# Optimization experiments

Hardware: AMD Instinct MI355X
Metric: run time of the kernel (lower is better)

The kernel has to match this reference:

```python
import jax, jax.numpy as jnp
import numpy as np

B, N, D, H, C = 16, 512, 256, 8, 16
DK = D // H  # per-head dim


def gelu(x):
    return jax.nn.gelu(x, approximate=False)  # torch F.gelu default (erf)


def mha(x, Wq, Wk, Wv, Wo):
    # x: [N, D] treated as a length-N token sequence; standard scaled-dot MHA
    n = x.shape[0]
    q = (x @ Wq).reshape(n, H, DK)
    k = (x @ Wk).reshape(n, H, DK)
    v = (x @ Wv).reshape(n, H, DK)
    scores = jnp.einsum('nhd,mhd->hnm', q, k) / jnp.sqrt(jnp.asarray(DK, x.dtype))
    attn = jax.nn.softmax(scores, axis=-1)
    out = jnp.einsum('hnm,mhd->nhd', attn, v).reshape(n, H * DK)
    return out @ Wo


def setup_inputs() -> dict:
    key = jax.random.key(0)
    ks = jax.random.split(key, 16)
    scale = 1.0 / np.sqrt(D)
    w = lambda i, shape: jax.random.normal(ks[i], shape, jnp.float32) * scale
    return {
        'embeddings': jax.random.normal(ks[0], (B, N, D), jnp.float32),
        'labels': jax.random.randint(ks[1], (B, N), 0, C),
        'Wq0': w(2, (D, D)), 'Wk0': w(3, (D, D)), 'Wv0': w(4, (D, D)), 'Wo0': w(5, (D, D)),
        'Wq1': w(6, (D, D)), 'Wk1': w(7, (D, D)), 'Wv1': w(8, (D, D)), 'Wo1': w(9, (D, D)),
        'res_W': w(10, (D, D)), 'res_b': jnp.zeros((D,), jnp.float32),
        'ff_W1': w(11, (2 * D, D)), 'ff_b1': jnp.zeros((D,), jnp.float32),
        'ff_W2': w(12, (D, D)), 'ff_b2': jnp.zeros((D,), jnp.float32),
    }


def reference(embeddings, labels, Wq0, Wk0, Wv0, Wo0, Wq1, Wk1, Wv1, Wo1,
              res_W, res_b, ff_W1, ff_b1, ff_W2, ff_b2):
    # one-hot class membership; torch.unique over randint labels == arange(C)
    onehot = (labels[..., None] == jnp.arange(C)).astype(jnp.float32)  # [B,N,C]

    def episode(e, m):
        # e: [N, D]  m: [N, C]
        x = mha(e, Wq0, Wk0, Wv0, Wo0)
        x = gelu(x)
        x = mha(x, Wq1, Wk1, Wv1, Wo1)
        aggr = gelu(jnp.mean(x, axis=0))          # [D]  set-level summary
        aggr = aggr @ res_W + res_b               # res_linear
        e2 = jnp.concatenate([jnp.broadcast_to(aggr, (N, D)), e], axis=1)  # [N,2D]
        e2 = gelu(e2)
        e2 = gelu(e2 @ ff_W1 + ff_b1) @ ff_W2 + ff_b2  # ff_linear -> [N,D]
        # pairwise sample similarities with self-exclusion
        S = e2 @ e2.T                              # [N,N]
        S = S * (1.0 - jnp.eye(N, dtype=S.dtype))
        counts = jnp.sum(m, axis=0)                # [C]
        norm = counts[None, :] - m                 # leave-one-out class size [N,C]
        return (S.T @ m) / norm                    # per-class masked mean -> [N,C]

    return jax.vmap(episode)(embeddings, onehot)
```

## Files before the change

kernel.cpp:

```cpp
#include <hip/hip_runtime.h>

#define BB 16
#define NN 512
#define DD 256
#define HH 8
#define CC 16

typedef unsigned short u16;
using short8 = __attribute__((ext_vector_type(8))) short;
using f32x4  = __attribute__((ext_vector_type(4))) float;

__device__ __forceinline__ float gelu_f(float x) {
    return 0.5f * x * (1.0f + erff(x * 0.70710678118654752f));
}
__device__ __forceinline__ u16 f2bf(float f) {
    unsigned int u = __float_as_uint(f);
    unsigned int r = u + 0x7FFFu + ((u >> 16) & 1u);
    return (u16)(r >> 16);
}
__device__ __forceinline__ void gld16(const u16* g, const u16* l) {
    __builtin_amdgcn_global_load_lds(
        (const __attribute__((address_space(1))) unsigned int*)g,
        (__attribute__((address_space(3))) unsigned int*)l, 16, 0, 0);
}

#define QSCALE 0.25505412f

template<int ACT, int HAS_B, int HAS_T, int OUT_F32>
__global__ __launch_bounds__(256) void gemm64(
    const u16* __restrict__ A, const u16* __restrict__ W,
    u16* __restrict__ O, float* __restrict__ OF,
    const float* __restrict__ bias, const float* __restrict__ tvec)
{
    __shared__ __align__(16) u16 As[64 * 32];
    __shared__ __align__(16) u16 Bs[64 * 32];
    const int tid = threadIdx.x, wave = tid >> 6, lane = tid & 63;
    const int col = lane & 15, quad = lane >> 4;
    const int mbase = blockIdx.x * 64;
    const int nbase = blockIdx.y * 64;
    const int srow = lane >> 2, skk = (lane & 3) * 8;
    const int mh = (wave & 1) * 32, nh = (wave >> 1) * 32;

    f32x4 acc[2][2];
#pragma unroll
    for (int i = 0; i < 2; ++i)
#pragma unroll
        for (int j = 0; j < 2; ++j) acc[i][j] = (f32x4){0.f, 0.f, 0.f, 0.f};

    for (int k0 = 0; k0 < DD; k0 += 32) {
        gld16(A + (size_t)(mbase + wave * 16 + srow) * DD + k0 + skk, &As[wave * 512]);
        gld16(W + (size_t)(nbase + wave * 16 + srow) * DD + k0 + skk, &Bs[wave * 512]);
        __syncthreads();
        short8 af[2], bfr[2];
#pragma unroll
        for (int i = 0; i < 2; ++i) af[i]  = *(const short8*)&As[(mh + i * 16 + col) * 32 + quad * 8];
#pragma unroll
        for (int j = 0; j < 2; ++j) bfr[j] = *(const short8*)&Bs[(nh + j * 16 + col) * 32 + quad * 8];
#pragma unroll
        for (int i = 0; i < 2; ++i)
#pragma unroll
            for (int j = 0; j < 2; ++j)
                acc[i][j] = __builtin_amdgcn_mfma_f32_16x16x32_bf16(af[i], bfr[j], acc[i][j], 0, 0, 0);
        __syncthreads();
    }

    const int b = mbase >> 9;
#pragma unroll
    for (int i = 0; i < 2; ++i) {
#pragma unroll
        for (int j = 0; j < 2; ++j) {
            const int ccol = nbase + nh + j * 16 + col;
#pragma unroll
            for (int r = 0; r < 4; ++r) {
                const int crow = mbase + mh + i * 16 + quad * 4 + r;
                float v = acc[i][j][r];
                if (HAS_B) v += bias[ccol];
                if (HAS_T) v += tvec[b * DD + ccol];
                if (ACT)   v = gelu_f(v);
                if (OUT_F32) OF[(size_t)crow * DD + ccol] = v;
                else         O[(size_t)crow * DD + ccol] = f2bf(v);
            }
        }
    }
}

__global__ __launch_bounds__(256) void gemm_qkv(
    const u16* __restrict__ A,
    const u16* __restrict__ W0, const u16* __restrict__ W1, const u16* __restrict__ W2,
    u16* __restrict__ O0, u16* __restrict__ O1, u16* __restrict__ O2)
{
    __shared__ __align__(16) u16 As[64 * 32];
    __shared__ __align__(16) u16 Bs[64 * 32];
    const int tid = threadIdx.x, wave = tid >> 6, lane = tid & 63;
    const int col = lane & 15, quad = lane >> 4;
    const int mbase = blockIdx.x * 64;
    const int sel = blockIdx.y >> 2;
    const int nbase = (blockIdx.y & 3) * 64;
    const u16* W = (sel == 0) ? W0 : ((sel == 1) ? W1 : W2);
    u16* O = (sel == 0) ? O0 : ((sel == 1) ? O1 : O2);
    const int srow = lane >> 2, skk = (lane & 3) * 8;
    const int mh = (wave & 1) * 32, nh = (wave >> 1) * 32;

    f32x4 acc[2][2];
#pragma unroll
    for (int i = 0; i < 2; ++i)
#pragma unroll
        for (int j = 0; j < 2; ++j) acc[i][j] = (f32x4){0.f, 0.f, 0.f, 0.f};

    for (int k0 = 0; k0 < DD; k0 += 32) {
        gld16(A + (size_t)(mbase + wave * 16 + srow) * DD + k0 + skk, &As[wave * 512]);
        gld16(W + (size_t)(nbase + wave * 16 + srow) * DD + k0 + skk, &Bs[wave * 512]);
        __syncthreads();
        short8 af[2], bfr[2];
#pragma unroll
        for (int i = 0; i < 2; ++i) af[i]  = *(const short8*)&As[(mh + i * 16 + col) * 32 + quad * 8];
#pragma unroll
        for (int j = 0; j < 2; ++j) bfr[j] = *(const short8*)&Bs[(nh + j * 16 + col) * 32 + quad * 8];
#pragma unroll
        for (int i = 0; i < 2; ++i)
#pragma unroll
            for (int j = 0; j < 2; ++j)
                acc[i][j] = __builtin_amdgcn_mfma_f32_16x16x32_bf16(af[i], bfr[j], acc[i][j], 0, 0, 0);
        __syncthreads();
    }

    const int b = mbase >> 9;
#pragma unroll
    for (int i = 0; i < 2; ++i) {
#pragma unroll
        for (int j = 0; j < 2; ++j) {
            const int ccol = nbase + nh + j * 16 + col;
            const int tok0 = (mbase & 511) + mh + i * 16 + quad * 4;
            const int head = ccol >> 5, dk = ccol & 31;
            if (sel == 2) {
                ushort4 pk;
                pk.x = f2bf(acc[i][j][0]); pk.y = f2bf(acc[i][j][1]);
                pk.z = f2bf(acc[i][j][2]); pk.w = f2bf(acc[i][j][3]);
                *(ushort4*)&O[(((size_t)b * HH + head) * 32 + dk) * NN + tok0] = pk;
            } else {
#pragma unroll
                for (int r = 0; r < 4; ++r) {
                    float v = acc[i][j][r];
                    if (sel == 0) v *= QSCALE;
                    O[(((size_t)b * HH + head) * NN + tok0 + r) * 32 + dk] = f2bf(v);
                }
            }
        }
    }
}

template<int COLSUM>
__global__ __launch_bounds__(256) void attn_mfma(
    const u16* __restrict__ Qh, const u16* __restrict__ Kh,
    const u16* __restrict__ VT, u16* __restrict__ O,
    float* __restrict__ partial)
{
    __shared__ __align__(16) u16 Vt[32 * 520];
    __shared__ __align__(16) u16 Pc[4][16 * 32];
    __shared__ float cs[4][32];
    const int tid = threadIdx.x, wave = tid >> 6, lane = tid & 63;
    const int col = lane & 15, quad = lane >> 4;
    const int gid = blockIdx.x;
    const int qb = gid >> 7, bh = gid & 127;
    const int q0 = qb * 64 + wave * 16;

    const u16* vsrc = VT + (size_t)bh * 32 * NN;
#pragma unroll
    for (int i = 0; i < 8; ++i) {
        const int row = wave + i * 4;
        gld16(vsrc + (size_t)row * NN + lane * 8, &Vt[row * 520]);
    }
    const short8 aq = *(const short8*)(Qh + ((size_t)bh * NN + q0 + col) * 32 + quad * 8);
    __syncthreads();

    const u16* ksrc = Kh + (size_t)bh * NN * 32;
    float l[4] = {0.f, 0.f, 0.f, 0.f};
    f32x4 oacc[2];
    oacc[0] = (f32x4){0.f, 0.f, 0.f, 0.f};
    oacc[1] = (f32x4){0.f, 0.f, 0.f, 0.f};

    for (int g = 0; g < 16; ++g) {
#pragma unroll
        for (int k2 = 0; k2 < 2; ++k2) {
            const int kt = g * 2 + k2;
            const short8 bk = *(const short8*)(ksrc + (size_t)(kt * 16 + col) * 32 + quad * 8);
            f32x4 z = {0.f, 0.f, 0.f, 0.f};
            const f32x4 s = __builtin_amdgcn_mfma_f32_16x16x32_bf16(aq, bk, z, 0, 0, 0);
#pragma unroll
            for (int r = 0; r < 4; ++r) {
                const float p = exp2f(s[r]);
                l[r] += p;
                Pc[wave][(quad * 4 + r) * 32 + k2 * 16 + col] = f2bf(p);
            }
        }
        const short8 ap = *(const short8*)&Pc[wave][col * 32 + quad * 8];
#pragma unroll
        for (int nt = 0; nt < 2; ++nt) {
            const short8 bv = *(const short8*)&Vt[(nt * 16 + col) * 520 + g * 32 + quad * 8];
            oacc[nt] = __builtin_amdgcn_mfma_f32_16x16x32_bf16(ap, bv, oacc[nt], 0, 0, 0);
        }
    }
#pragma unroll
    for (int r = 0; r < 4; ++r) {
        l[r] += __shfl_xor(l[r], 1, 64);
        l[r] += __shfl_xor(l[r], 2, 64);
        l[r] += __shfl_xor(l[r], 4, 64);
        l[r] += __shfl_xor(l[r], 8, 64);
    }
    if (COLSUM) {
        float sv[2] = {0.f, 0.f};
#pragma unroll
        for (int nt = 0; nt < 2; ++nt) {
#pragma unroll
            for (int r = 0; r < 4; ++r) sv[nt] += oacc[nt][r] / l[r];
            sv[nt] += __shfl_xor(sv[nt], 16, 64);
            sv[nt] += __shfl_xor(sv[nt], 32, 64);
        }
        if (lane < 16) { cs[wave][col] = sv[0]; cs[wave][16 + col] = sv[1]; }
        __syncthreads();
        if (tid < 32)
            partial[(size_t)(bh * 8 + qb) * 32 + tid] =
                cs[0][tid] + cs[1][tid] + cs[2][tid] + cs[3][tid];
    } else {
        const int b = bh >> 3, h = bh & 7;
        u16* obase = O + ((size_t)b * NN) * DD + h * 32;
#pragma unroll
        for (int nt = 0; nt < 2; ++nt)
#pragma unroll
            for (int r = 0; r < 4; ++r)
                obase[(size_t)(q0 + quad * 4 + r) * DD + nt * 16 + col] = f2bf(oacc[nt][r] / l[r]);
    }
}

__global__ __launch_bounds__(256) void convert_all(
    const float* __restrict__ e, u16* __restrict__ E, u16* __restrict__ G,
    const float* s0, const float* s1, const float* s2, const float* s3,
    const float* s4, const float* s5, const float* s6, const float* s7,
    const float* s8, u16* __restrict__ Wt)
{
    const int bx = blockIdx.x;
    if (bx < 2048) {
        const size_t i = ((size_t)bx * 256 + threadIdx.x) * 4;
        const float4 v = *(const float4*)(e + i);
        ushort4 ev, gv;
        ev.x = f2bf(v.x); ev.y = f2bf(v.y); ev.z = f2bf(v.z); ev.w = f2bf(v.w);
        gv.x = f2bf(gelu_f(v.x)); gv.y = f2bf(gelu_f(v.y));
        gv.z = f2bf(gelu_f(v.z)); gv.w = f2bf(gelu_f(v.w));
        *(ushort4*)(E + i) = ev;
        *(ushort4*)(G + i) = gv;
    } else {
        const int w = bx - 2048;
        const int my = w >> 4, kb = (w & 15) * 16;
        const int n = threadIdx.x;
        const float* S;
        switch (my) {
            case 0: S = s0; break; case 1: S = s1; break; case 2: S = s2; break;
            case 3: S = s3; break; case 4: S = s4; break; case 5: S = s5; break;
            case 6: S = s6; break; case 7: S = s7; break; default: S = s8; break;
        }
        u16* Dst = Wt + (size_t)my * 65536;
        for (int r = 0; r < 16; ++r) {
            const int k = kb + r;
            Dst[(size_t)n * 256 + k] = f2bf(S[(size_t)k * 256 + n]);
        }
    }
}

__device__ __forceinline__ float mv256(const float* __restrict__ a,
                                       const float* __restrict__ W, int d)
{
    float acc[8] = {0.f, 0.f, 0.f, 0.f, 0.f, 0.f, 0.f, 0.f};
    for (int k = 0; k < 256; k += 8) {
#pragma unroll
        for (int j = 0; j < 8; ++j)
            acc[j] += a[k + j] * W[(size_t)(k + j) * 256 + d];
    }
    return ((acc[0] + acc[1]) + (acc[2] + acc[3])) + ((acc[4] + acc[5]) + (acc[6] + acc[7]));
}

__global__ __launch_bounds__(256) void aggr_v2(
    const float* __restrict__ partial, const float* __restrict__ Wo1f,
    const float* __restrict__ resW, const float* __restrict__ resb,
    const float* __restrict__ W1, const int* __restrict__ labels,
    float* __restrict__ tvec, float* __restrict__ counts)
{
    const int b = blockIdx.x, d = threadIdx.x;
    __shared__ float a0[256], a1[256], a2[256];
    __shared__ int hist[CC];
    if (d < CC) hist[d] = 0;
    const int h = d >> 5, d32 = d & 31;
    float s = 0.f;
#pragma unroll
    for (int qb = 0; qb < 8; ++qb)
        s += partial[(size_t)(((b * 8 + h) * 8) + qb) * 32 + d32];
    a0[d] = s * (1.0f / NN);
    __syncthreads();
    atomicAdd(&hist[labels[b * NN + d]], 1);
    atomicAdd(&hist[labels[b * NN + 256 + d]], 1);
    a1[d] = gelu_f(mv256(a0, Wo1f, d));
    __syncthreads();
    a2[d] = gelu_f(mv256(a1, resW, d) + resb[d]);
    __syncthreads();
    tvec[b * 256 + d] = mv256(a2, W1, d);
    if (d < CC) counts[b * CC + d] = (float)hist[d];
}

__global__ __launch_bounds__(256) void classsum_v2(
    const float* __restrict__ F, const int* __restrict__ labels,
    float* __restrict__ g)
{
    const int b = blockIdx.x, dch = blockIdx.y;
    const int t = threadIdx.x, w = t >> 6, lane = t & 63;
    __shared__ int lab[NN];
    __shared__ float gs[4][CC][64];
    lab[t] = labels[b * NN + t];
    lab[t + 256] = labels[b * NN + t + 256];
    __syncthreads();
    float acc[CC];
#pragma unroll
    for (int c = 0; c < CC; ++c) acc[c] = 0.f;
    const float* Fb = F + (size_t)b * NN * DD + dch * 64 + lane;
#pragma unroll 4
    for (int n = w * 128; n < w * 128 + 128; ++n) {
        const float v = Fb[(size_t)n * DD];
        const int lb = lab[n];
#pragma unroll
        for (int c = 0; c < CC; ++c) acc[c] += (lb == c) ? v : 0.f;
    }
#pragma unroll
    for (int c = 0; c < CC; ++c) gs[w][c][lane] = acc[c];
    __syncthreads();
#pragma unroll
    for (int i = 0; i < 4; ++i) {
        const int c = w * 4 + i;
        g[((size_t)b * CC + c) * DD + dch * 64 + lane] =
            gs[0][c][lane] + gs[1][c][lane] + gs[2][c][lane] + gs[3][c][lane];
    }
}

__global__ __launch_bounds__(256) void out_kernel(
    const float* __restrict__ F, const int* __restrict__ labels,
    const float* __restrict__ g, const float* __restrict__ counts,
    float* __restrict__ out)
{
    const int b = blockIdx.y;
    const int wave = threadIdx.x >> 6, lane = threadIdx.x & 63;
    const int n = blockIdx.x * 4 + wave;
    const float* fn = F + ((size_t)b * NN + n) * DD;
    const float* gb = g + (size_t)b * CC * DD;
    float fv[4];
#pragma unroll
    for (int i = 0; i < 4; ++i) fv[i] = fn[lane * 4 + i];
    float selfdot = 0.f;
#pragma unroll
    for (int i = 0; i < 4; ++i) selfdot += fv[i] * fv[i];
    float accs[CC];
#pragma unroll
    for (int c = 0; c < CC; ++c) {
        float sacc = 0.f;
#pragma unroll
        for (int i = 0; i < 4; ++i) sacc += fv[i] * gb[c * DD + lane * 4 + i];
        accs[c] = sacc;
    }
    for (int off = 32; off; off >>= 1) {
        selfdot += __shfl_xor(selfdot, off, 64);
#pragma unroll
        for (int c = 0; c < CC; ++c) accs[c] += __shfl_xor(accs[c], off, 64);
    }
    if (lane < CC) {
        const int c = lane;
        const int same = (labels[b * NN + n] == c) ? 1 : 0;
        const float num = accs[c] - (same ? selfdot : 0.f);
        const float den = counts[b * CC + c] - (float)same;
        out[((size_t)b * NN + n) * CC + c] = num / den;
    }
}

extern "C" void kernel_launch(void* const* d_in, const int* in_sizes, int n_in,
                              void* d_out, int out_size, void* d_ws, size_t ws_size,
                              hipStream_t stream)
{
    const float* emb    = (const float*)d_in[0];
    const int*   labels = (const int*)  d_in[1];
    const float* Wo1f = (const float*)d_in[9];
    const float* resW = (const float*)d_in[10];
    const float* resb = (const float*)d_in[11];
    const float* ffW1 = (const float*)d_in[12];
    const float* ffb1 = (const float*)d_in[13];
    const float* ffb2 = (const float*)d_in[15];
    float* out = (float*)d_out;

    const size_t SBE = (size_t)BB * NN * DD;
    u16* BUF0 = (u16*)d_ws;
    u16* BUF1 = BUF0 + SBE;
    u16* BUF2 = BUF1 + SBE;
    u16* BUF3 = BUF2 + SBE;
    u16* BUF4 = BUF3 + SBE;
    u16* BUF5 = BUF4 + SBE;
    u16* Wt   = BUF5 + SBE;
    float* F      = (float*)(Wt + 9 * 65536);
    float* tvec   = F + SBE;
    float* partial= tvec + BB * 256;
    float* gsum   = partial + 128 * 8 * 32;
    float* counts = gsum + (size_t)BB * CC * DD;

    convert_all<<<2048 + 144, 256, 0, stream>>>(
        emb, BUF0, BUF1,
        (const float*)d_in[2], (const float*)d_in[3], (const float*)d_in[4],
        (const float*)d_in[5], (const float*)d_in[6], (const float*)d_in[7],
        (const float*)d_in[8], ffW1 + 256 * 256, (const float*)d_in[14], Wt);
    gemm_qkv<<<dim3(128, 12), 256, 0, stream>>>(
        BUF0, Wt, Wt + 65536, Wt + 2 * 65536, BUF2, BUF3, BUF4);
    attn_mfma<0><<<1024, 256, 0, stream>>>(BUF2, BUF3, BUF4, BUF5, nullptr);
    gemm64<1,0,0,0><<<dim3(128, 4), 256, 0, stream>>>(
        BUF5, Wt + 3 * 65536, BUF0, nullptr, nullptr, nullptr);
    gemm_qkv<<<dim3(128, 12), 256, 0, stream>>>(
        BUF0, Wt + 4 * 65536, Wt + 5 * 65536, Wt + 6 * 65536, BUF2, BUF3, BUF4);
    attn_mfma<1><<<1024, 256, 0, stream>>>(BUF2, BUF3, BUF4, nullptr, partial);
    aggr_v2<<<BB, 256, 0, stream>>>(partial, Wo1f, resW, resb, ffW1, labels, tvec, counts);
    gemm64<1,1,1,0><<<dim3(128, 4), 256, 0, stream>>>(
        BUF1, Wt + 7 * 65536, BUF3, nullptr, ffb1, tvec);
    gemm64<0,1,0,1><<<dim3(128, 4), 256, 0, stream>>>(
        BUF3, Wt + 8 * 65536, nullptr, F, ffb2, nullptr);
    classsum_v2<<<dim3(BB, 4), 256, 0, stream>>>(F, labels, gsum);
    out_kernel<<<dim3(128, BB), 256, 0, stream>>>(F, labels, gsum, counts, out);
}
```

Baseline: 213.0 us.

## Fuse aggregation into attention tail and class sums into FF2 GEMM epilogue

```diff
diff --git a/kernel.cpp b/kernel.cpp
--- a/kernel.cpp
+++ b/kernel.cpp
@@ -26,11 +26,24 @@
 
 #define QSCALE 0.25505412f
 
-template<int ACT, int HAS_B, int HAS_T, int OUT_F32>
+__device__ __forceinline__ float mv256(const float* __restrict__ a,
+                                       const float* __restrict__ W, int d)
+{
+    float acc[8] = {0.f, 0.f, 0.f, 0.f, 0.f, 0.f, 0.f, 0.f};
+    for (int k = 0; k < 256; k += 8) {
+#pragma unroll
+        for (int j = 0; j < 8; ++j)
+            acc[j] += a[k + j] * W[(size_t)(k + j) * 256 + d];
+    }
+    return ((acc[0] + acc[1]) + (acc[2] + acc[3])) + ((acc[4] + acc[5]) + (acc[6] + acc[7]));
+}
+
+template<int ACT, int HAS_B, int HAS_T, int OUT_F32, int CS>
 __global__ __launch_bounds__(256) void gemm64(
     const u16* __restrict__ A, const u16* __restrict__ W,
     u16* __restrict__ O, float* __restrict__ OF,
-    const float* __restrict__ bias, const float* __restrict__ tvec)
+    const float* __restrict__ bias, const float* __restrict__ tvec,
+    const int* __restrict__ labels, float* __restrict__ gsum)
 {
     __shared__ __align__(16) u16 As[64 * 32];
     __shared__ __align__(16) u16 Bs[64 * 32];
@@ -65,21 +78,66 @@
     }
 
     const int b = mbase >> 9;
-#pragma unroll
-    for (int i = 0; i < 2; ++i) {
-#pragma unroll
-        for (int j = 0; j < 2; ++j) {
-            const int ccol = nbase + nh + j * 16 + col;
-#pragma unroll
-            for (int r = 0; r < 4; ++r) {
-                const int crow = mbase + mh + i * 16 + quad * 4 + r;
-                float v = acc[i][j][r];
-                if (HAS_B) v += bias[ccol];
-                if (HAS_T) v += tvec[b * DD + ccol];
-                if (ACT)   v = gelu_f(v);
-                if (OUT_F32) OF[(size_t)crow * DD + ccol] = v;
-                else         O[(size_t)crow * DD + ccol] = f2bf(v);
+    if constexpr (!CS) {
+#pragma unroll
+        for (int i = 0; i < 2; ++i) {
+#pragma unroll
+            for (int j = 0; j < 2; ++j) {
+                const int ccol = nbase + nh + j * 16 + col;
+#pragma unroll
+                for (int r = 0; r < 4; ++r) {
+                    const int crow = mbase + mh + i * 16 + quad * 4 + r;
+                    float v = acc[i][j][r];
+                    if (HAS_B) v += bias[ccol];
+                    if (HAS_T) v += tvec[b * DD + ccol];
+                    if (ACT)   v = gelu_f(v);
+                    if (OUT_F32) OF[(size_t)crow * DD + ccol] = v;
+                    else         O[(size_t)crow * DD + ccol] = f2bf(v);
+                }
             }
+        }
+    } else {
+        __shared__ float Fs[64][65];
+        __shared__ float gs[4][CC][64];
+        __shared__ int lab2[64];
+        if (tid < 64) lab2[tid] = labels[mbase + tid];
+#pragma unroll
+        for (int i = 0; i < 2; ++i) {
+#pragma unroll
+            for (int j = 0; j < 2; ++j) {
+                const int lcol = nh + j * 16 + col;
+                const int ccol = nbase + lcol;
+#pragma unroll
+                for (int r = 0; r < 4; ++r) {
+                    const int lrow = mh + i * 16 + quad * 4 + r;
+                    float v = acc[i][j][r];
+                    if (HAS_B) v += bias[ccol];
+                    if (HAS_T) v += tvec[b * DD + ccol];
+                    if (ACT)   v = gelu_f(v);
+                    OF[(size_t)(mbase + lrow) * DD + ccol] = v;
+                    Fs[lrow][lcol] = v;
+                }
+            }
+        }
+        __syncthreads();
+        float a[CC];
+#pragma unroll
+        for (int c = 0; c < CC; ++c) a[c] = 0.f;
+#pragma unroll
+        for (int n = 0; n < 16; ++n) {
+            const float v = Fs[wave * 16 + n][lane];
+            const int lb = lab2[wave * 16 + n];
+#pragma unroll
+            for (int c = 0; c < CC; ++c) a[c] += (lb == c) ? v : 0.f;
+        }
+#pragma unroll
+        for (int c = 0; c < CC; ++c) gs[wave][c][lane] = a[c];
+        __syncthreads();
+#pragma unroll
+        for (int i = 0; i < 4; ++i) {
+            const int c = wave * 4 + i;
+            atomicAdd(&gsum[((size_t)b * CC + c) * DD + nbase + lane],
+                      gs[0][c][lane] + gs[1][c][lane] + gs[2][c][lane] + gs[3][c][lane]);
         }
     }
 }
@@ -153,7 +211,11 @@
 __global__ __launch_bounds__(256) void attn_mfma(
     const u16* __restrict__ Qh, const u16* __restrict__ Kh,
     const u16* __restrict__ VT, u16* __restrict__ O,
-    float* __restrict__ partial)
+    float* __restrict__ partial,
+    const float* __restrict__ Wo1f, const float* __restrict__ resW,
+    const float* __restrict__ resb, const float* __restrict__ W1,
+    const int* __restrict__ labels, float* __restrict__ tvec,
+    float* __restrict__ counts, int* __restrict__ flags)
 {
     __shared__ __align__(16) u16 Vt[32 * 520];
     __shared__ __align__(16) u16 Pc[4][16 * 32];
@@ -218,9 +280,38 @@
         }
         if (lane < 16) { cs[wave][col] = sv[0]; cs[wave][16 + col] = sv[1]; }
         __syncthreads();
+        const int b = bh >> 3;
         if (tid < 32)
             partial[(size_t)(bh * 8 + qb) * 32 + tid] =
                 cs[0][tid] + cs[1][tid] + cs[2][tid] + cs[3][tid];
+        __threadfence();
+        __syncthreads();
+        __shared__ int isLast;
+        if (tid == 0) isLast = (atomicAdd(&flags[b], 1) == 63);
+        __syncthreads();
+        if (!isLast) return;
+        __threadfence();
+        float* a0 = (float*)Vt;
+        float* a1 = a0 + 256;
+        float* a2 = a1 + 256;
+        int* hist = (int*)(a2 + 256);
+        const int d = tid;
+        if (d < CC) hist[d] = 0;
+        const int hh = d >> 5, d32 = d & 31;
+        float s = 0.f;
+#pragma unroll
+        for (int q8 = 0; q8 < 8; ++q8)
+            s += partial[(size_t)(((b * 8 + hh) * 8) + q8) * 32 + d32];
+        a0[d] = s * (1.0f / NN);
+        __syncthreads();
+        atomicAdd(&hist[labels[b * NN + d]], 1);
+        atomicAdd(&hist[labels[b * NN + 256 + d]], 1);
+        a1[d] = gelu_f(mv256(a0, Wo1f, d));
+        __syncthreads();
+        a2[d] = gelu_f(mv256(a1, resW, d) + resb[d]);
+        __syncthreads();
+        tvec[b * 256 + d] = mv256(a2, W1, d);
+        if (d < CC) counts[b * CC + d] = (float)hist[d];
     } else {
         const int b = bh >> 3, h = bh & 7;
         u16* obase = O + ((size_t)b * NN) * DD + h * 32;
@@ -236,7 +327,8 @@
     const float* __restrict__ e, u16* __restrict__ E, u16* __restrict__ G,
     const float* s0, const float* s1, const float* s2, const float* s3,
     const float* s4, const float* s5, const float* s6, const float* s7,
-    const float* s8, u16* __restrict__ Wt)
+    const float* s8, u16* __restrict__ Wt,
+    float* __restrict__ gsum, int* __restrict__ flags)
 {
     const int bx = blockIdx.x;
     if (bx < 2048) {
@@ -248,7 +340,7 @@
         gv.z = f2bf(gelu_f(v.z)); gv.w = f2bf(gelu_f(v.w));
         *(ushort4*)(E + i) = ev;
         *(ushort4*)(G + i) = gv;
-    } else {
+    } else if (bx < 2192) {
         const int w = bx - 2048;
         const int my = w >> 4, kb = (w & 15) * 16;
         const int n = threadIdx.x;
@@ -263,78 +355,11 @@
             const int k = kb + r;
             Dst[(size_t)n * 256 + k] = f2bf(S[(size_t)k * 256 + n]);
         }
-    }
-}
-
-__device__ __forceinline__ float mv256(const float* __restrict__ a,
-                                       const float* __restrict__ W, int d)
-{
-    float acc[8] = {0.f, 0.f, 0.f, 0.f, 0.f, 0.f, 0.f, 0.f};
-    for (int k = 0; k < 256; k += 8) {
-#pragma unroll
-        for (int j = 0; j < 8; ++j)
-            acc[j] += a[k + j] * W[(size_t)(k + j) * 256 + d];
-    }
-    return ((acc[0] + acc[1]) + (acc[2] + acc[3])) + ((acc[4] + acc[5]) + (acc[6] + acc[7]));
-}
-
-__global__ __launch_bounds__(256) void aggr_v2(
-    const float* __restrict__ partial, const float* __restrict__ Wo1f,
-    const float* __restrict__ resW, const float* __restrict__ resb,
-    const float* __restrict__ W1, const int* __restrict__ labels,
-    float* __restrict__ tvec, float* __restrict__ counts)
-{
-    const int b = blockIdx.x, d = threadIdx.x;
-    __shared__ float a0[256], a1[256], a2[256];
-    __shared__ int hist[CC];
-    if (d < CC) hist[d] = 0;
-    const int h = d >> 5, d32 = d & 31;
-    float s = 0.f;
-#pragma unroll
-    for (int qb = 0; qb < 8; ++qb)
-        s += partial[(size_t)(((b * 8 + h) * 8) + qb) * 32 + d32];
-    a0[d] = s * (1.0f / NN);
-    __syncthreads();
-    atomicAdd(&hist[labels[b * NN + d]], 1);
-    atomicAdd(&hist[labels[b * NN + 256 + d]], 1);
-    a1[d] = gelu_f(mv256(a0, Wo1f, d));
-    __syncthreads();
-    a2[d] = gelu_f(mv256(a1, resW, d) + resb[d]);
-    __syncthreads();
-    tvec[b * 256 + d] = mv256(a2, W1, d);
-    if (d < CC) counts[b * CC + d] = (float)hist[d];
-}
-
-__global__ __launch_bounds__(256) void classsum_v2(
-    const float* __restrict__ F, const int* __restrict__ labels,
-    float* __restrict__ g)
-{
-    const int b = blockIdx.x, dch = blockIdx.y;
-    const int t = threadIdx.x, w = t >> 6, lane = t & 63;
-    __shared__ int lab[NN];
-    __shared__ float gs[4][CC][64];
-    lab[t] = labels[b * NN + t];
-    lab[t + 256] = labels[b * NN + t + 256];
-    __syncthreads();
-    float acc[CC];
-#pragma unroll
-    for (int c = 0; c < CC; ++c) acc[c] = 0.f;
-    const float* Fb = F + (size_t)b * NN * DD + dch * 64 + lane;
-#pragma unroll 4
-    for (int n = w * 128; n < w * 128 + 128; ++n) {
-        const float v = Fb[(size_t)n * DD];
-        const int lb = lab[n];
-#pragma unroll
-        for (int c = 0; c < CC; ++c) acc[c] += (lb == c) ? v : 0.f;
-    }
-#pragma unroll
-    for (int c = 0; c < CC; ++c) gs[w][c][lane] = acc[c];
-    __syncthreads();
-#pragma unroll
-    for (int i = 0; i < 4; ++i) {
-        const int c = w * 4 + i;
-        g[((size_t)b * CC + c) * DD + dch * 64 + lane] =
-            gs[0][c][lane] + gs[1][c][lane] + gs[2][c][lane] + gs[3][c][lane];
+    } else {
+        const int z = bx - 2192;
+        const float4 zz = {0.f, 0.f, 0.f, 0.f};
+        *(float4*)(gsum + (size_t)z * 1024 + threadIdx.x * 4) = zz;
+        if (z == 0 && threadIdx.x < BB) flags[threadIdx.x] = 0;
     }
 }
 
@@ -403,25 +428,29 @@
     float* partial= tvec + BB * 256;
     float* gsum   = partial + 128 * 8 * 32;
     float* counts = gsum + (size_t)BB * CC * DD;
-
-    convert_all<<<2048 + 144, 256, 0, stream>>>(
+    int*   flags  = (int*)(counts + BB * CC);
+
+    convert_all<<<2048 + 144 + 64, 256, 0, stream>>>(
         emb, BUF0, BUF1,
         (const float*)d_in[2], (const float*)d_in[3], (const float*)d_in[4],
         (const float*)d_in[5], (const float*)d_in[6], (const float*)d_in[7],
-        (const float*)d_in[8], ffW1 + 256 * 256, (const float*)d_in[14], Wt);
+        (const float*)d_in[8], ffW1 + 256 * 256, (const float*)d_in[14], Wt,
+        gsum, flags);
     gemm_qkv<<<dim3(128, 12), 256, 0, stream>>>(
         BUF0, Wt, Wt + 65536, Wt + 2 * 65536, BUF2, BUF3, BUF4);
-    attn_mfma<0><<<1024, 256, 0, stream>>>(BUF2, BUF3, BUF4, BUF5, nullptr);
-    gemm64<1,0,0,0><<<dim3(128, 4), 256, 0, stream>>>(
-        BUF5, Wt + 3 * 65536, BUF0, nullptr, nullptr, nullptr);
+    attn_mfma<0><<<1024, 256, 0, stream>>>(
+        BUF2, BUF3, BUF4, BUF5, nullptr,
+        nullptr, nullptr, nullptr, nullptr, nullptr, nullptr, nullptr, nullptr);
+    gemm64<1,0,0,0,0><<<dim3(128, 4), 256, 0, stream>>>(
+        BUF5, Wt + 3 * 65536, BUF0, nullptr, nullptr, nullptr, nullptr, nullptr);
     gemm_qkv<<<dim3(128, 12), 256, 0, stream>>>(
         BUF0, Wt + 4 * 65536, Wt + 5 * 65536, Wt + 6 * 65536, BUF2, BUF3, BUF4);
-    attn_mfma<1><<<1024, 256, 0, stream>>>(BUF2, BUF3, BUF4, nullptr, partial);
-    aggr_v2<<<BB, 256, 0, stream>>>(partial, Wo1f, resW, resb, ffW1, labels, tvec, counts);
-    gemm64<1,1,1,0><<<dim3(128, 4), 256, 0, stream>>>(
-        BUF1, Wt + 7 * 65536, BUF3, nullptr, ffb1, tvec);
-    gemm64<0,1,0,1><<<dim3(128, 4), 256, 0, stream>>>(
-        BUF3, Wt + 8 * 65536, nullptr, F, ffb2, nullptr);
-    classsum_v2<<<dim3(BB, 4), 256, 0, stream>>>(F, labels, gsum);
+    attn_mfma<1><<<1024, 256, 0, stream>>>(
+        BUF2, BUF3, BUF4, nullptr, partial,
+        Wo1f, resW, resb, ffW1, labels, tvec, counts, flags);
+    gemm64<1,1,1,0,0><<<dim3(128, 4), 256, 0, stream>>>(
+        BUF1, Wt + 7 * 65536, BUF3, nullptr, ffb1, tvec, nullptr, nullptr);
+    gemm64<0,1,0,1,1><<<dim3(128, 4), 256, 0, stream>>>(
+        BUF3, Wt + 8 * 65536, nullptr, F, ffb2, nullptr, labels, gsum);
     out_kernel<<<dim3(128, BB), 256, 0, stream>>>(F, labels, gsum, counts, out);
 }
```

New measurement: 259.7 us. 21.9% more time.
